# Optimization experiments

Measured on AMD Instinct MI355X. Metric: run time of the kernel, lower is better.

The kernel has to match this reference:

```python
import jax, jax.numpy as jnp
import numpy as np

B = 4194304   # batch of generated samples
C = 100       # number of classifier classes

def setup_inputs() -> dict:
    key = jax.random.key(0)
    logits = jax.random.normal(key, (B, C), dtype=jnp.float32)
    return {"logits": logits, "batch_size": B}

def reference(logits, batch_size):
    # argmax over classes -> predicted label per sample  [B]
    labels = jnp.argmax(logits, axis=1)
    # histogram of labels (replaces CPU Counter)          [C]
    counts = jnp.zeros((logits.shape[1],), dtype=jnp.float32).at[labels].add(1.0)
    p = counts / jnp.float32(batch_size)
    # entropy: -sum p*log2(p), skipping empty bins (Counter only iterates present labels)
    ent_terms = jnp.where(p > 0, p * (jnp.log(jnp.maximum(p, 1e-30)) / jnp.log(jnp.float32(2.0))), 0.0)
    loss = -jnp.sum(ent_terms)
    return loss
```

## Files before the change

kernel.cpp:

```cpp
#include <hip/hip_runtime.h>

#define NCLASS 100
#define TROWS 64
#define CHUNKS 25

typedef float fx4 __attribute__((ext_vector_type(4)));

__global__ __launch_bounds__(64) void argmax_hist_kernel(
    const fx4* __restrict__ g4,
    unsigned int* __restrict__ counts,
    int nrows)
{
    __shared__ float2 part[TROWS * CHUNKS];
    __shared__ unsigned int lhist[NCLASS];

    const int tid = threadIdx.x;
    #pragma unroll
    for (int i = tid; i < NCLASS; i += TROWS) lhist[i] = 0u;
    __syncthreads();

    const int ntiles = nrows / TROWS;
    fx4 stg[CHUNKS];

    int tile = blockIdx.x;
    if (tile < ntiles) {
        const size_t b4 = (size_t)tile * (TROWS * CHUNKS);
        #pragma unroll
        for (int i = 0; i < CHUNKS; ++i)
            stg[i] = __builtin_nontemporal_load(&g4[b4 + i * TROWS + tid]);
    }

    while (tile < ntiles) {
        #pragma unroll
        for (int i = 0; i < CHUNKS; ++i) {
            const fx4 v = stg[i];
            float m = v.x; int ci = 0;
            if (v.y > m) { m = v.y; ci = 1; }
            if (v.z > m) { m = v.z; ci = 2; }
            if (v.w > m) { m = v.w; ci = 3; }
            const int f = i * TROWS + tid;
            const int c = f % CHUNKS;
            part[f] = make_float2(m, (float)(4 * c + ci));
        }

        const int ntile = tile + gridDim.x;
        if (ntile < ntiles) {
            const size_t b4 = (size_t)ntile * (TROWS * CHUNKS);
            #pragma unroll
            for (int i = 0; i < CHUNKS; ++i)
                stg[i] = __builtin_nontemporal_load(&g4[b4 + i * TROWS + tid]);
        }

        __syncthreads();

        const float2* rp = &part[tid * CHUNKS];
        float best = -__builtin_huge_valf();
        float bcol = 0.0f;
        #pragma unroll
        for (int j = 0; j < CHUNKS; ++j) {
            const float2 v = rp[j];
            if (v.x > best) { best = v.x; bcol = v.y; }
        }
        atomicAdd(&lhist[(int)bcol], 1u);

        __syncthreads();
        tile = ntile;
    }

    #pragma unroll
    for (int i = tid; i < NCLASS; i += TROWS) {
        unsigned int c = lhist[i];
        if (c) atomicAdd(&counts[i], c);
    }
}

__global__ __launch_bounds__(128) void entropy_kernel(
    const unsigned int* __restrict__ counts,
    float* __restrict__ out,
    float invB)
{
    __shared__ float partial[128];
    const int t = threadIdx.x;
    float term = 0.0f;
    if (t < NCLASS) {
        float c = (float)counts[t];
        if (c > 0.0f) {
            float p = c * invB;
            term = p * (logf(p) * 1.4426950408889634f);
        }
    }
    partial[t] = term;
    __syncthreads();
    #pragma unroll
    for (int s = 64; s > 0; s >>= 1) {
        if (t < s) partial[t] += partial[t + s];
        __syncthreads();
    }
    if (t == 0) out[0] = -partial[0];
}

extern "C" void kernel_launch(void* const* d_in, const int* in_sizes, int n_in,
                              void* d_out, int out_size, void* d_ws, size_t ws_size,
                              hipStream_t stream)
{
    const float* logits = (const float*)d_in[0];
    const int nrows = in_sizes[0] / NCLASS;

    unsigned int* counts = (unsigned int*)d_ws;
    (void)hipMemsetAsync(counts, 0, NCLASS * sizeof(unsigned int), stream);

    const int grid = 4096;
    argmax_hist_kernel<<<grid, TROWS, 0, stream>>>(
        (const fx4*)logits, counts, nrows);

    entropy_kernel<<<1, 128, 0, stream>>>(counts, (float*)d_out, 1.0f / (float)nrows);
}
```

Before: 310.1 us.

## Stream logits directly into double-buffered LDS via global_load_lds

```diff
diff --git a/kernel.cpp b/kernel.cpp
--- a/kernel.cpp
+++ b/kernel.cpp
@@ -11,7 +11,7 @@
     unsigned int* __restrict__ counts,
     int nrows)
 {
-    __shared__ float2 part[TROWS * CHUNKS];
+    __shared__ fx4 buf[2][CHUNKS * TROWS];
     __shared__ unsigned int lhist[NCLASS];
 
     const int tid = threadIdx.x;
@@ -20,51 +20,50 @@
     __syncthreads();
 
     const int ntiles = nrows / TROWS;
-    fx4 stg[CHUNKS];
+    const int stride = gridDim.x;
+
+    #define ISSUE_TILE(b_, tile_)                                               \
+        {                                                                       \
+            const fx4* src = g4 + (size_t)(tile_) * (CHUNKS * TROWS) + tid;     \
+            _Pragma("unroll")                                                   \
+            for (int i = 0; i < CHUNKS; ++i) {                                  \
+                __builtin_amdgcn_global_load_lds(                               \
+                    (const __attribute__((address_space(1))) void*)(src + i * TROWS), \
+                    (__attribute__((address_space(3))) void*)(&buf[(b_)][i * TROWS]), \
+                    16, 0, 0);                                                  \
+            }                                                                   \
+        }
 
     int tile = blockIdx.x;
-    if (tile < ntiles) {
-        const size_t b4 = (size_t)tile * (TROWS * CHUNKS);
-        #pragma unroll
-        for (int i = 0; i < CHUNKS; ++i)
-            stg[i] = __builtin_nontemporal_load(&g4[b4 + i * TROWS + tid]);
-    }
+    int b = 0;
+    if (tile < ntiles) ISSUE_TILE(0, tile);
 
     while (tile < ntiles) {
-        #pragma unroll
-        for (int i = 0; i < CHUNKS; ++i) {
-            const fx4 v = stg[i];
-            float m = v.x; int ci = 0;
-            if (v.y > m) { m = v.y; ci = 1; }
-            if (v.z > m) { m = v.z; ci = 2; }
-            if (v.w > m) { m = v.w; ci = 3; }
-            const int f = i * TROWS + tid;
-            const int c = f % CHUNKS;
-            part[f] = make_float2(m, (float)(4 * c + ci));
+        const int nxt = tile + stride;
+        const bool has_next = (nxt < ntiles);
+        if (has_next) {
+            ISSUE_TILE(b ^ 1, nxt);
+            asm volatile("s_waitcnt vmcnt(25)" ::: "memory");
+        } else {
+            asm volatile("s_waitcnt vmcnt(0)" ::: "memory");
         }
+        __builtin_amdgcn_sched_barrier(0);
 
-        const int ntile = tile + gridDim.x;
-        if (ntile < ntiles) {
-            const size_t b4 = (size_t)ntile * (TROWS * CHUNKS);
-            #pragma unroll
-            for (int i = 0; i < CHUNKS; ++i)
-                stg[i] = __builtin_nontemporal_load(&g4[b4 + i * TROWS + tid]);
-        }
-
-        __syncthreads();
-
-        const float2* rp = &part[tid * CHUNKS];
+        const fx4* rp = &buf[b][tid * CHUNKS];
         float best = -__builtin_huge_valf();
-        float bcol = 0.0f;
+        int bcol = 0;
         #pragma unroll
         for (int j = 0; j < CHUNKS; ++j) {
-            const float2 v = rp[j];
-            if (v.x > best) { best = v.x; bcol = v.y; }
+            const fx4 v = rp[j];
+            if (v.x > best) { best = v.x; bcol = 4 * j + 0; }
+            if (v.y > best) { best = v.y; bcol = 4 * j + 1; }
+            if (v.z > best) { best = v.z; bcol = 4 * j + 2; }
+            if (v.w > best) { best = v.w; bcol = 4 * j + 3; }
         }
-        atomicAdd(&lhist[(int)bcol], 1u);
+        atomicAdd(&lhist[bcol], 1u);
 
-        __syncthreads();
-        tile = ntile;
+        b ^= 1;
+        tile = nxt;
     }
 
     #pragma unroll
@@ -72,6 +71,7 @@
         unsigned int c = lhist[i];
         if (c) atomicAdd(&counts[i], c);
     }
+    #undef ISSUE_TILE
 }
 
 __global__ __launch_bounds__(128) void entropy_kernel(
@@ -109,7 +109,7 @@
     unsigned int* counts = (unsigned int*)d_ws;
     (void)hipMemsetAsync(counts, 0, NCLASS * sizeof(unsigned int), stream);
 
-    const int grid = 4096;
+    const int grid = 768;
     argmax_hist_kernel<<<grid, TROWS, 0, stream>>>(
         (const fx4*)logits, counts, nrows);
 
```

Result: faster. 286.3 us (-7.7%).
